# Kernel optimization log

Measured on AMD Instinct MI355X. Metric: run time of the kernel, lower is better.

The kernel has to match this reference:

```python
import jax, jax.numpy as jnp
import numpy as np

B, S, D = 2, 1024, 4096
H, KVH = 32, 8
HD = D // H          # 128
N_REP = H // KVH     # 4
R = 2                # LoRA rank


def setup_inputs() -> dict:
    key = jax.random.key(0)
    ks = jax.random.split(key, 10)
    sc = 0.02
    x = jax.random.normal(ks[0], (B, S, D), jnp.float32)
    wq = jax.random.normal(ks[1], (D, H * HD), jnp.float32) * sc
    wk = jax.random.normal(ks[2], (D, KVH * HD), jnp.float32) * sc
    wv = jax.random.normal(ks[3], (D, KVH * HD), jnp.float32) * sc
    wo = jax.random.normal(ks[4], (H * HD, D), jnp.float32) * sc
    lora_q_a = jax.random.normal(ks[5], (D, R), jnp.float32) * sc
    lora_q_b = jax.random.normal(ks[6], (R, H * HD), jnp.float32) * sc
    lora_v_a = jax.random.normal(ks[7], (D, R), jnp.float32) * sc
    lora_v_b = jax.random.normal(ks[8], (R, KVH * HD), jnp.float32) * sc
    # RoPE frequencies: freqs_cis[t, i] = exp(1j * t * 10000^(-2i/HD))
    inv_freq = 1.0 / (10000.0 ** (jnp.arange(0, HD, 2, dtype=jnp.float32) / HD))  # [HD/2]
    t = jnp.arange(S, dtype=jnp.float32)
    ang = jnp.outer(t, inv_freq)                      # [S, HD/2]
    freqs_cos = jnp.cos(ang)
    freqs_sin = jnp.sin(ang)
    # causal additive mask [1, 1, S, S]
    mask = jnp.triu(jnp.full((S, S), -1e9, jnp.float32), k=1)[None, None]
    return {"x": x, "wq": wq, "wk": wk, "wv": wv, "wo": wo,
            "lora_q_a": lora_q_a, "lora_q_b": lora_q_b,
            "lora_v_a": lora_v_a, "lora_v_b": lora_v_b,
            "freqs_cos": freqs_cos, "freqs_sin": freqs_sin,
            "mask": mask, "start_pos": 0}


def _rope(t, cos, sin):
    # t: [B, S, h, HD]; pairs (even, odd) are (real, imag) of complex halves
    b, s, h, hd = t.shape
    tr = t.reshape(b, s, h, hd // 2, 2)
    a, bb = tr[..., 0], tr[..., 1]
    c = cos[None, :, None, :]
    sn = sin[None, :, None, :]
    out = jnp.stack([a * c - bb * sn, a * sn + bb * c], axis=-1)
    return out.reshape(b, s, h, hd)


def reference(x, wq, wk, wv, wo, lora_q_a, lora_q_b, lora_v_a, lora_v_b,
              freqs_cos, freqs_sin, mask, start_pos):
    # projections + LoRA (note: original Lora_layer applies NO scaling in forward)
    xq = x @ wq + (x @ lora_q_a) @ lora_q_b            # [B,S,H*HD]
    xk = x @ wk                                         # [B,S,KVH*HD]
    xv = x @ wv + (x @ lora_v_a) @ lora_v_b             # [B,S,KVH*HD]
    xq = xq.reshape(B, S, H, HD)
    xk = xk.reshape(B, S, KVH, HD)
    xv = xv.reshape(B, S, KVH, HD)
    xq = _rope(xq, freqs_cos, freqs_sin)
    xk = _rope(xk, freqs_cos, freqs_sin)
    # repeat_kv (GQA expansion): [B,S,KVH,HD] -> [B,S,H,HD]
    k = jnp.repeat(xk, N_REP, axis=2)
    v = jnp.repeat(xv, N_REP, axis=2)
    # attention
    scores = jnp.einsum('bshd,bthd->bhst', xq, k) / np.sqrt(HD).astype(np.float32)
    scores = scores + mask
    probs = jax.nn.softmax(scores.astype(jnp.float32), axis=-1).astype(xq.dtype)
    out = jnp.einsum('bhst,bthd->bshd', probs, v)       # [B,S,H,HD]
    out = out.reshape(B, S, H * HD) @ wo                # [B,S,D]
    return out
```

## Files before the change

kernel.cpp:

```cpp
#include <hip/hip_runtime.h>
#include <stdint.h>

#define B_ 2
#define S_ 1024
#define D_ 4096
#define H_ 32
#define KVH_ 8
#define HD_ 128

typedef short short8 __attribute__((ext_vector_type(8)));
typedef float floatx4 __attribute__((ext_vector_type(4)));

__device__ __forceinline__ ushort f2bf(float f) {
  union { float f; uint32_t u; } v; v.f = f;
  return (ushort)((v.u + 0x7FFFu + ((v.u >> 16) & 1u)) >> 16);
}
__device__ __forceinline__ float bf2f(ushort u) {
  union { uint32_t x; float f; } v; v.x = ((uint32_t)u) << 16; return v.f;
}

__device__ __forceinline__ void gload16(const void* g, void* l) {
  __builtin_amdgcn_global_load_lds((__attribute__((address_space(1))) void*)g,
                                   (__attribute__((address_space(3))) void*)l,
                                   16, 0, 0);
}

__global__ __launch_bounds__(256) void k_cvtlora(const float* __restrict__ x,
                                                 const float* __restrict__ qa,
                                                 const float* __restrict__ va,
                                                 ushort* __restrict__ xb,
                                                 float* __restrict__ xa) {
  const int row = blockIdx.x, t = threadIdx.x;
  const float* xr = x + (size_t)row * D_;
  ushort* xo = xb + (size_t)row * D_;
  float a0 = 0, a1 = 0, a2 = 0, a3 = 0;
#pragma unroll
  for (int it = 0; it < 4; it++) {
    const int i = it * 1024 + t * 4;
    float4 v = *(const float4*)(xr + i);
    ushort o4[4] = {f2bf(v.x), f2bf(v.y), f2bf(v.z), f2bf(v.w)};
    *(uint2*)(xo + i) = *(uint2*)o4;
    float4 q0 = *(const float4*)(qa + 2 * i);
    float4 q1 = *(const float4*)(qa + 2 * i + 4);
    float4 w0 = *(const float4*)(va + 2 * i);
    float4 w1 = *(const float4*)(va + 2 * i + 4);
    a0 += v.x * q0.x + v.y * q0.z + v.z * q1.x + v.w * q1.z;
    a1 += v.x * q0.y + v.y * q0.w + v.z * q1.y + v.w * q1.w;
    a2 += v.x * w0.x + v.y * w0.z + v.z * w1.x + v.w * w1.z;
    a3 += v.x * w0.y + v.y * w0.w + v.z * w1.y + v.w * w1.w;
  }
#pragma unroll
  for (int off = 32; off; off >>= 1) {
    a0 += __shfl_down(a0, off, 64);
    a1 += __shfl_down(a1, off, 64);
    a2 += __shfl_down(a2, off, 64);
    a3 += __shfl_down(a3, off, 64);
  }
  __shared__ float red[4][4];
  const int w = t >> 6, lane = t & 63;
  if (lane == 0) { red[w][0] = a0; red[w][1] = a1; red[w][2] = a2; red[w][3] = a3; }
  __syncthreads();
  if (t < 4)
    xa[(size_t)row * 4 + t] = red[0][t] + red[1][t] + red[2][t] + red[3][t];
}

__global__ __launch_bounds__(256) void k_trw4(const float* __restrict__ wq,
                                              const float* __restrict__ wo,
                                              const float* __restrict__ wk,
                                              const float* __restrict__ wv,
                                              ushort* __restrict__ oq,
                                              ushort* __restrict__ oo,
                                              ushort* __restrict__ ok,
                                              ushort* __restrict__ ov) {
  const int z = blockIdx.z;
  const bool narrow = (z >= 2);
  if (narrow && blockIdx.x >= 16) return;
  const float* in = (z == 0) ? wq : (z == 1) ? wo : (z == 2) ? wk : wv;
  ushort* out = (z == 0) ? oq : (z == 1) ? oo : (z == 2) ? ok : ov;
  const int in_stride = narrow ? 1024 : 4096;
  __shared__ float t[64][65];
  const int n0 = blockIdx.x * 64, k0 = blockIdx.y * 64;
  const int c4 = (threadIdx.x & 15) * 4, r = threadIdx.x >> 4;
#pragma unroll
  for (int rr = 0; rr < 64; rr += 16) {
    float4 v = *(const float4*)&in[(size_t)(k0 + r + rr) * in_stride + n0 + c4];
    t[r + rr][c4] = v.x; t[r + rr][c4 + 1] = v.y;
    t[r + rr][c4 + 2] = v.z; t[r + rr][c4 + 3] = v.w;
  }
  __syncthreads();
#pragma unroll
  for (int rr = 0; rr < 64; rr += 16) {
    const int n = r + rr;
    ushort o4[4] = {f2bf(t[c4][n]), f2bf(t[c4 + 1][n]),
                    f2bf(t[c4 + 2][n]), f2bf(t[c4 + 3][n])};
    *(uint2*)&out[(size_t)(n0 + n) * 4096 + k0 + c4] = *(uint2*)o4;
  }
}

#define GBAR __builtin_amdgcn_s_barrier()
#define VMCNT0 asm volatile("s_waitcnt vmcnt(0)" ::: "memory")
#define VMCNT6 asm volatile("s_waitcnt vmcnt(6)" ::: "memory")

#define QSTG(T, SB) do {                                                     \
    const ushort* ga_ = A + (size_t)(m0 + w * 16 + qsr) * Kz + (T) * 64 + qsc; \
    char* la_ = qlds + (SB) * 65536 + w * 2048;                              \
    gload16(ga_, la_); gload16(ga_ + 8 * Kz, la_ + 1024);                    \
    _Pragma("unroll") for (int u_ = 0; u_ < 3; u_++) {                       \
      const ushort* gb_ = Bt + (size_t)(n0 + u_ * 128 + w * 16 + qsr) * Kz   \
                          + (T) * 64 + qsc;                                  \
      char* lb_ = qlds + (SB) * 65536 + 16384 + u_ * 16384 + w * 2048;       \
      gload16(gb_, lb_); gload16(gb_ + 8 * Kz, lb_ + 1024);                  \
    }                                                                        \
  } while (0)

__global__ __launch_bounds__(512, 2) void k_gemmq(const ushort* __restrict__ A,
                                                  const ushort* __restrict__ Bt,
                                                  ushort* __restrict__ Qb,
                                                  ushort* __restrict__ Kb,
                                                  ushort* __restrict__ Vt,
                                                  const float* __restrict__ xa,
                                                  const float* __restrict__ qb,
                                                  const float* __restrict__ vb,
                                                  const float* __restrict__ fcos,
                                                  const float* __restrict__ fsin) {
  __shared__ char qlds[131072];
  const int flat = blockIdx.y * 16 + blockIdx.x;
  const int swz_id = (flat & 7) * 32 + (flat >> 3);
  const int m0 = (swz_id >> 4) * 128, n0 = (swz_id & 15) * 384;
  const int tid = threadIdx.x, lane = tid & 63, w = tid >> 6;
  const int wr = w >> 2, wc = w & 3;
  const int lr = lane & 15, g = lane >> 4;
  const int swz = (lr & 7) * 16;
  const size_t Kz = 4096;
  const int qsr = lane >> 3;
  const int qsc = ((lane & 7) ^ (qsr & 7)) * 8;

  floatx4 acc[4][6] = {};
  short8 af[4][2], bfr[6][2];

  QSTG(0, 0);
  VMCNT0;
  GBAR;

  for (int t = 0; t < 64; ++t) {
    const int bu = t & 1;
    if (t + 1 < 64) QSTG(t + 1, bu ^ 1);
    const char* ab_ = qlds + bu * 65536 + (wr * 64 + lr) * 128;
#pragma unroll
    for (int fr = 0; fr < 4; fr++)
#pragma unroll
      for (int ks = 0; ks < 2; ks++)
        af[fr][ks] = *(const short8*)(ab_ + fr * 2048 + (((ks * 4 + g) * 16) ^ swz));
    const char* bb_ = qlds + bu * 65536 + 16384 + (wc * 32 + lr) * 128;
#pragma unroll
    for (int u = 0; u < 3; u++)
#pragma unroll
      for (int e = 0; e < 2; e++)
#pragma unroll
        for (int ks = 0; ks < 2; ks++)
          bfr[u * 2 + e][ks] = *(const short8*)(bb_ + u * 16384 + e * 2048 +
                                                (((ks * 4 + g) * 16) ^ swz));
    __builtin_amdgcn_s_setprio(1);
#pragma unroll
    for (int fr = 0; fr < 4; fr++)
#pragma unroll
      for (int u = 0; u < 6; u++)
#pragma unroll
        for (int ks = 0; ks < 2; ks++)
          acc[fr][u] = __builtin_amdgcn_mfma_f32_16x16x32_bf16(
              af[fr][ks], bfr[u][ks], acc[fr][u], 0, 0, 0);
    __builtin_amdgcn_s_setprio(0);
    VMCNT0;
    GBAR;
  }

#pragma unroll
  for (int fr = 0; fr < 4; fr++) {
    const int mb = m0 + wr * 64 + fr * 16 + g * 4;
    const int bb = mb >> 10, s0 = mb & 1023;
    float4 xa4[4];
#pragma unroll
    for (int r = 0; r < 4; r++) xa4[r] = *(const float4*)&xa[(size_t)(mb + r) * 4];
#pragma unroll
    for (int j = 0; j < 3; j++)
#pragma unroll
      for (int e = 0; e < 2; e++) {
        const int n = n0 + j * 128 + wc * 32 + e * 16 + lr;
        if (n < 5120) {
          const bool lq = (n < 4096);
          float b0 = 0.f, b1 = 0.f;
          if (lq) { b0 = qb[n]; b1 = qb[4096 + n]; }
          const int p = (n & 127) >> 1;
          const bool even = !(n & 1);
          const int d = n & 127;
          ushort* dst = lq ? (Qb + ((size_t)(bb * H_ + (n >> 7)) * S_) * HD_ + d)
                           : (Kb + ((size_t)(bb * KVH_ + ((n - 4096) >> 7)) * S_) * HD_ + d);
#pragma unroll
          for (int r = 0; r < 4; r++) {
            float cc = acc[fr][j * 2 + e][r];
            if (lq) cc += xa4[r].x * b0 + xa4[r].y * b1;
            float pv = __shfl_xor(cc, 1, 64);
            const int s = s0 + r;
            float c = fcos[s * 64 + p], sn = fsin[s * 64 + p];
            float o = even ? (cc * c - pv * sn) : (cc * c + pv * sn);
            dst[(size_t)s * HD_] = f2bf(o);
          }
        } else {
          const int vcol = n - 5120;
          const float b0 = vb[vcol], b1 = vb[1024 + vcol];
          ushort v4[4];
#pragma unroll
          for (int r = 0; r < 4; r++)
            v4[r] = f2bf(acc[fr][j * 2 + e][r] + xa4[r].z * b0 + xa4[r].w * b1);
          *(uint2*)&Vt[(size_t)((bb * 8 + (vcol >> 7)) * 128 + (vcol & 127)) * 1024 + s0] =
              *(uint2*)v4;
        }
      }
  }
}

#define OSTG(T, SB) do {                                                     \
    const ushort* ga_ = A + (size_t)(m0 + w * 16 + osr) * Kz + (T) * 64 + osc; \
    char* la_ = olds + (SB) * 49152 + w * 2048;                              \
    gload16(ga_, la_); gload16(ga_ + 8 * Kz, la_ + 1024);                    \
    _Pragma("unroll") for (int u_ = 0; u_ < 2; u_++) {                       \
      const ushort* gb_ = Bt + (size_t)(n0 + u_ * 128 + w * 16 + osr) * Kz + (T) * 64 + osc; \
      char* lb_ = olds + (SB) * 49152 + 16384 + u_ * 16384 + w * 2048;       \
      gload16(gb_, lb_); gload16(gb_ + 8 * Kz, lb_ + 1024);                  \
    }                                                                        \
  } while (0)

#define OTILE(T, RB) do {                                                    \
    if ((T) + 2 < 64) OSTG((T) + 2, ((RB) + 2) % 3);                         \
    const char* ab_ = olds + (RB) * 49152 + (wr * 64 + lr) * 128;            \
    _Pragma("unroll") for (int fr = 0; fr < 4; fr++)                         \
    _Pragma("unroll") for (int ks = 0; ks < 2; ks++)                         \
      af[fr][ks] = *(const short8*)(ab_ + fr * 2048 + (((ks * 4 + g) * 16) ^ swz)); \
    const char* bb_ = olds + (RB) * 49152 + 16384 + (wc * 32 + lr) * 128;    \
    _Pragma("unroll") for (int u_ = 0; u_ < 2; u_++)                         \
    _Pragma("unroll") for (int e_ = 0; e_ < 2; e_++)                         \
    _Pragma("unroll") for (int ks = 0; ks < 2; ks++)                         \
      bfr[u_ * 2 + e_][ks] = *(const short8*)(bb_ + u_ * 16384 + e_ * 2048 + (((ks * 4 + g) * 16) ^ swz)); \
    __builtin_amdgcn_s_setprio(1);                                           \
    _Pragma("unroll") for (int fr = 0; fr < 4; fr++)                         \
    _Pragma("unroll") for (int u_ = 0; u_ < 4; u_++)                         \
    _Pragma("unroll") for (int ks = 0; ks < 2; ks++)                         \
      acc[fr][u_] = __builtin_amdgcn_mfma_f32_16x16x32_bf16(                 \
          af[fr][ks], bfr[u_][ks], acc[fr][u_], 0, 0, 0);                    \
    __builtin_amdgcn_s_setprio(0);                                           \
    if ((T) + 2 < 64) { VMCNT6; } else { VMCNT0; }                           \
    GBAR;                                                                    \
  } while (0)

__global__ __launch_bounds__(512, 2) void k_gemmo(const ushort* __restrict__ A,
                                                  const ushort* __restrict__ Bt,
                                                  float* __restrict__ C) {
  __shared__ char olds[147456];
  const int flat = blockIdx.y * 16 + blockIdx.x;
  const int swz_id = (flat & 7) * 32 + (flat >> 3);
  const int m0 = (swz_id >> 4) * 128, n0 = (swz_id & 15) * 256;
  const int tid = threadIdx.x, lane = tid & 63, w = tid >> 6;
  const int wr = w >> 2, wc = w & 3;
  const int lr = lane & 15, g = lane >> 4;
  const int swz = (lr & 7) * 16;
  const size_t Kz = 4096;
  const int osr = lane >> 3;
  const int osc = ((lane & 7) ^ (osr & 7)) * 8;

  floatx4 acc[4][4] = {};
  short8 af[4][2], bfr[4][2];

  OSTG(0, 0); OSTG(1, 1);
  VMCNT6;
  GBAR;

  for (int tt = 0; tt < 63; tt += 3) {
    OTILE(tt + 0, 0);
    OTILE(tt + 1, 1);
    OTILE(tt + 2, 2);
  }
  OTILE(63, 0);

#pragma unroll
  for (int fr = 0; fr < 4; fr++) {
    const int mb = m0 + wr * 64 + fr * 16 + g * 4;
#pragma unroll
    for (int j = 0; j < 2; j++)
#pragma unroll
      for (int e = 0; e < 2; e++) {
        const int n = n0 + j * 128 + wc * 32 + e * 16 + lr;
#pragma unroll
        for (int r = 0; r < 4; r++)
          C[(size_t)(mb + r) * 4096 + n] = acc[fr][j * 2 + e][r];
      }
  }
}

#define FSTAGE(T, DB) do {                                                   \
    _Pragma("unroll") for (int i_ = 0; i_ < 4; i_++) {                       \
      gload16(Kg + (size_t)((T) * 64 + i_ * 16 + k_srow) * HD_ + k_scol,     \
              fls + (DB) * 16384 + i_ * 4096 + w * 1024);                    \
      gload16(Vg + (size_t)(i_ * 32 + v_srow) * S_ + (T) * 64 + v_scol,      \
              fls + 32768 + (DB) * 16384 + i_ * 4096 + w * 1024);            \
    }                                                                        \
  } while (0)

__global__ __launch_bounds__(256, 2) void k_flash(const ushort* __restrict__ Qb,
                                                  const ushort* __restrict__ Kb,
                                                  const ushort* __restrict__ Vt,
                                                  ushort* __restrict__ attn) {
  __shared__ char fls[81920];
  const int qblk = (gridDim.x - 1) - blockIdx.x;
  const int h = blockIdx.y, b = blockIdx.z;
  const int kvh = h >> 2;
  const int tid = threadIdx.x, w = tid >> 6, lane = tid & 63;
  const int lr = lane & 15, g = lane >> 4;
  const int swz = (lr & 7) * 16;
  const int qra = qblk * 128 + w * 16;
  const ushort* Qrow = Qb + ((size_t)(b * H_ + h) * S_ + qra + lr) * HD_;
  short8 qfa[4], qfb[4];
#pragma unroll
  for (int ks = 0; ks < 4; ks++) {
    qfa[ks] = *(const short8*)(Qrow + ks * 32 + g * 8);
    qfb[ks] = *(const short8*)(Qrow + 64 * HD_ + ks * 32 + g * 8);
  }
  const ushort* Kg = Kb + (size_t)(b * KVH_ + kvh) * S_ * HD_;
  const ushort* Vg = Vt + (size_t)(b * KVH_ + kvh) * HD_ * S_;
  char* Pw = fls + 65536 + w * 4096;
  const int q7 = lr & 7;
  const int k_srow = tid >> 4;
  const int k_scol = ((tid & 15) ^ (k_srow & 7)) * 8;
  const int v_srow = tid >> 3;
  const int v_scol = ((tid & 7) ^ (v_srow & 7)) * 8;
  const float scale = 0.088388347648318447f;

  float m_a = -1e30f, l_a = 0.f, m_b = -1e30f, l_b = 0.f;
  floatx4 oa[8] = {}, ob[8] = {};
  const int nt = 2 * qblk + 2;
  const int lastA = 2 * qblk;

  FSTAGE(0, 0);
  VMCNT0;
  GBAR;

  for (int t = 0; t < nt; t++) {
    const int cur = t & 1;
    if (t + 1 < nt) FSTAGE(t + 1, cur ^ 1);
    const char* Kl = fls + cur * 16384;
    const char* Vl = fls + 32768 + cur * 16384;
    if (t <= lastA) {
      floatx4 s4[4] = {};
      __builtin_amdgcn_s_setprio(1);
#pragma unroll
      for (int mf = 0; mf < 4; mf++) {
        const char* Krow = Kl + (mf * 16 + lr) * 256;
#pragma unroll
        for (int ks = 0; ks < 4; ks++) {
          short8 kf = *(const short8*)(Krow + (((ks * 4 + g) * 16) ^ swz));
          s4[mf] = __builtin_amdgcn_mfma_f32_16x16x32_bf16(kf, qfa[ks], s4[mf], 0, 0, 0);
        }
      }
      __builtin_amdgcn_s_setprio(0);
      float tm = -1e30f;
      if (t == lastA) {
#pragma unroll
        for (int mf = 0; mf < 4; mf++)
#pragma unroll
          for (int r = 0; r < 4; r++) {
            int kv = t * 64 + mf * 16 + g * 4 + r;
            float v = (kv > qra + lr) ? -1e30f : s4[mf][r] * scale;
            s4[mf][r] = v; tm = fmaxf(tm, v);
          }
      } else {
#pragma unroll
        for (int mf = 0; mf < 4; mf++)
#pragma unroll
          for (int r = 0; r < 4; r++) {
            float v = s4[mf][r] * scale;
            s4[mf][r] = v; tm = fmaxf(tm, v);
          }
      }
      tm = fmaxf(tm, __shfl_xor(tm, 16, 64));
      tm = fmaxf(tm, __shfl_xor(tm, 32, 64));
      float m_new = fmaxf(m_a, tm);
      float corr = __expf(m_a - m_new);
      float rs = 0.f;
#pragma unroll
      for (int mf = 0; mf < 4; mf++)
#pragma unroll
        for (int r = 0; r < 4; r++) {
          float p = __expf(s4[mf][r] - m_new);
          s4[mf][r] = p; rs += p;
        }
      rs += __shfl_xor(rs, 16, 64);
      rs += __shfl_xor(rs, 32, 64);
      l_a = l_a * corr + rs; m_a = m_new;
#pragma unroll
      for (int r = 0; r < 4; r++) {
        float cr = __shfl(corr, g * 4 + r, 64);
#pragma unroll
        for (int nf = 0; nf < 8; nf++) oa[nf][r] *= cr;
      }
#pragma unroll
      for (int mf = 0; mf < 4; mf++) {
        uint2 pv;
        pv.x = (uint32_t)f2bf(s4[mf][0]) | ((uint32_t)f2bf(s4[mf][1]) << 16);
        pv.y = (uint32_t)f2bf(s4[mf][2]) | ((uint32_t)f2bf(s4[mf][3]) << 16);
        *(uint2*)(Pw + lr * 128 + ((mf * 32 + g * 8) ^ (q7 << 4))) = pv;
      }
    }
    {
      floatx4 s4[4] = {};
      __builtin_amdgcn_s_setprio(1);
#pragma unroll
      for (int mf = 0; mf < 4; mf++) {
        const char* Krow = Kl + (mf * 16 + lr) * 256;
#pragma unroll
        for (int ks = 0; ks < 4; ks++) {
          short8 kf = *(const short8*)(Krow + (((ks * 4 + g) * 16) ^ swz));
          s4[mf] = __builtin_amdgcn_mfma_f32_16x16x32_bf16(kf, qfb[ks], s4[mf], 0, 0, 0);
        }
      }
      __builtin_amdgcn_s_setprio(0);
      float tm = -1e30f;
      if (t == nt - 1) {
#pragma unroll
        for (int mf = 0; mf < 4; mf++)
#pragma unroll
          for (int r = 0; r < 4; r++) {
            int kv = t * 64 + mf * 16 + g * 4 + r;
            float v = (kv > qra + 64 + lr) ? -1e30f : s4[mf][r] * scale;
            s4[mf][r] = v; tm = fmaxf(tm, v);
          }
      } else {
#pragma unroll
        for (int mf = 0; mf < 4; mf++)
#pragma unroll
          for (int r = 0; r < 4; r++) {
            float v = s4[mf][r] * scale;
            s4[mf][r] = v; tm = fmaxf(tm, v);
          }
      }
      tm = fmaxf(tm, __shfl_xor(tm, 16, 64));
      tm = fmaxf(tm, __shfl_xor(tm, 32, 64));
      float m_new = fmaxf(m_b, tm);
      float corr = __expf(m_b - m_new);
      float rs = 0.f;
#pragma unroll
      for (int mf = 0; mf < 4; mf++)
#pragma unroll
        for (int r = 0; r < 4; r++) {
          float p = __expf(s4[mf][r] - m_new);
          s4[mf][r] = p; rs += p;
        }
      rs += __shfl_xor(rs, 16, 64);
      rs += __shfl_xor(rs, 32, 64);
      l_b = l_b * corr + rs; m_b = m_new;
#pragma unroll
      for (int r = 0; r < 4; r++) {
        float cr = __shfl(corr, g * 4 + r, 64);
#pragma unroll
        for (int nf = 0; nf < 8; nf++) ob[nf][r] *= cr;
      }
#pragma unroll
      for (int mf = 0; mf < 4; mf++) {
        uint2 pv;
        pv.x = (uint32_t)f2bf(s4[mf][0]) | ((uint32_t)f2bf(s4[mf][1]) << 16);
        pv.y = (uint32_t)f2bf(s4[mf][2]) | ((uint32_t)f2bf(s4[mf][3]) << 16);
        *(uint2*)(Pw + 2048 + lr * 128 + ((mf * 32 + g * 8) ^ (q7 << 4))) = pv;
      }
    }
    __builtin_amdgcn_s_setprio(1);
#pragma unroll
    for (int ks2 = 0; ks2 < 2; ks2++) {
      short8 pb = *(const short8*)(Pw + 2048 + lr * 128 + ((ks2 * 64 + g * 16) ^ (q7 << 4)));
      short8 pa = pb;
      if (t <= lastA)
        pa = *(const short8*)(Pw + lr * 128 + ((ks2 * 64 + g * 16) ^ (q7 << 4)));
#pragma unroll
      for (int nf = 0; nf < 8; nf++) {
        short8 vf = *(const short8*)(Vl + (nf * 16 + lr) * 128 + (((ks2 * 4 + g) * 16) ^ swz));
        if (t <= lastA)
          oa[nf] = __builtin_amdgcn_mfma_f32_16x16x32_bf16(pa, vf, oa[nf], 0, 0, 0);
        ob[nf] = __builtin_amdgcn_mfma_f32_16x16x32_bf16(pb, vf, ob[nf], 0, 0, 0);
      }
    }
    __builtin_amdgcn_s_setprio(0);
    VMCNT0;
    GBAR;
  }
  const float linva = 1.0f / l_a, linvb = 1.0f / l_b;
  ushort* outp = attn + ((size_t)(b * S_) + qra) * 4096 + h * 128;
#pragma unroll
  for (int r = 0; r < 4; r++) {
    float lia = __shfl(linva, g * 4 + r, 64);
    float lib = __shfl(linvb, g * 4 + r, 64);
    ushort* orow = outp + (size_t)(g * 4 + r) * 4096;
#pragma unroll
    for (int nf = 0; nf < 8; nf++) {
      orow[nf * 16 + lr] = f2bf(oa[nf][r] * lia);
      orow[(size_t)64 * 4096 + nf * 16 + lr] = f2bf(ob[nf][r] * lib);
    }
  }
}

extern "C" void kernel_launch(void* const* d_in, const int* in_sizes, int n_in,
                              void* d_out, int out_size, void* d_ws, size_t ws_size,
                              hipStream_t stream) {
  (void)in_sizes; (void)n_in; (void)out_size; (void)ws_size;
  const float* x    = (const float*)d_in[0];
  const float* wq   = (const float*)d_in[1];
  const float* wk   = (const float*)d_in[2];
  const float* wv   = (const float*)d_in[3];
  const float* wo   = (const float*)d_in[4];
  const float* lqa  = (const float*)d_in[5];
  const float* lqb  = (const float*)d_in[6];
  const float* lva  = (const float*)d_in[7];
  const float* lvb  = (const float*)d_in[8];
  const float* fcos = (const float*)d_in[9];
  const float* fsin = (const float*)d_in[10];

  char* ws = (char*)d_ws;
  ushort* xb   = (ushort*)(ws + 0);
  ushort* wT   = (ushort*)(ws + 16777216);
  ushort* woT  = (ushort*)(ws + 67108864);
  ushort* Qb   = (ushort*)(ws + 150994944);
  ushort* Kb   = (ushort*)(ws + 167772160);
  ushort* Vt   = (ushort*)(ws + 171966464);
  ushort* attn = (ushort*)(ws + 176160768);
  float*  xa   = (float*) (ws + 192937984);

  k_cvtlora<<<2048, 256, 0, stream>>>(x, lqa, lva, xb, xa);
  k_trw4<<<dim3(64, 64, 4), 256, 0, stream>>>(
      wq, wo, wk, wv, wT, woT,
      wT + (size_t)4096 * 4096, wT + (size_t)5120 * 4096);
  k_gemmq<<<dim3(16, 16), 512, 0, stream>>>(xb, wT, Qb, Kb, Vt, xa, lqb, lvb,
                                            fcos, fsin);
  k_flash<<<dim3(8, 32, 2), 256, 0, stream>>>(Qb, Kb, Vt, attn);
  k_gemmo<<<dim3(16, 16), 512, 0, stream>>>(attn, woT, (float*)d_out);
}
```

Baseline: 291.8 us.

## Merge x-convert/LoRA into weight-transpose launch; double-buffer output GEMM

Folds the x-to-bf16 conversion and LoRA down-projection kernel into the weight transpose kernel as an extra grid z-slice, removing one launch and letting both run concurrently. Separately, the output projection GEMM goes from a triple-buffered LDS pipeline with partial vmcnt waits to a double-buffered one that waits for all loads each iteration. This cuts LDS from 144KB to 96KB per block, but the full vmcnt(0) wait exposes more global-load latency, because the prefetch is only one tile ahead.

```diff
diff --git a/kernel.cpp b/kernel.cpp
--- a/kernel.cpp
+++ b/kernel.cpp
@@ -25,54 +25,57 @@
                                    16, 0, 0);
 }
 
-__global__ __launch_bounds__(256) void k_cvtlora(const float* __restrict__ x,
-                                                 const float* __restrict__ qa,
-                                                 const float* __restrict__ va,
-                                                 ushort* __restrict__ xb,
-                                                 float* __restrict__ xa) {
-  const int row = blockIdx.x, t = threadIdx.x;
-  const float* xr = x + (size_t)row * D_;
-  ushort* xo = xb + (size_t)row * D_;
-  float a0 = 0, a1 = 0, a2 = 0, a3 = 0;
-#pragma unroll
-  for (int it = 0; it < 4; it++) {
-    const int i = it * 1024 + t * 4;
-    float4 v = *(const float4*)(xr + i);
-    ushort o4[4] = {f2bf(v.x), f2bf(v.y), f2bf(v.z), f2bf(v.w)};
-    *(uint2*)(xo + i) = *(uint2*)o4;
-    float4 q0 = *(const float4*)(qa + 2 * i);
-    float4 q1 = *(const float4*)(qa + 2 * i + 4);
-    float4 w0 = *(const float4*)(va + 2 * i);
-    float4 w1 = *(const float4*)(va + 2 * i + 4);
-    a0 += v.x * q0.x + v.y * q0.z + v.z * q1.x + v.w * q1.z;
-    a1 += v.x * q0.y + v.y * q0.w + v.z * q1.y + v.w * q1.w;
-    a2 += v.x * w0.x + v.y * w0.z + v.z * w1.x + v.w * w1.z;
-    a3 += v.x * w0.y + v.y * w0.w + v.z * w1.y + v.w * w1.w;
-  }
-#pragma unroll
-  for (int off = 32; off; off >>= 1) {
-    a0 += __shfl_down(a0, off, 64);
-    a1 += __shfl_down(a1, off, 64);
-    a2 += __shfl_down(a2, off, 64);
-    a3 += __shfl_down(a3, off, 64);
-  }
-  __shared__ float red[4][4];
-  const int w = t >> 6, lane = t & 63;
-  if (lane == 0) { red[w][0] = a0; red[w][1] = a1; red[w][2] = a2; red[w][3] = a3; }
-  __syncthreads();
-  if (t < 4)
-    xa[(size_t)row * 4 + t] = red[0][t] + red[1][t] + red[2][t] + red[3][t];
-}
-
-__global__ __launch_bounds__(256) void k_trw4(const float* __restrict__ wq,
+__global__ __launch_bounds__(256) void k_prep(const float* __restrict__ wq,
                                               const float* __restrict__ wo,
                                               const float* __restrict__ wk,
                                               const float* __restrict__ wv,
                                               ushort* __restrict__ oq,
                                               ushort* __restrict__ oo,
                                               ushort* __restrict__ ok,
-                                              ushort* __restrict__ ov) {
+                                              ushort* __restrict__ ov,
+                                              const float* __restrict__ x,
+                                              const float* __restrict__ qa,
+                                              const float* __restrict__ va,
+                                              ushort* __restrict__ xb,
+                                              float* __restrict__ xa) {
   const int z = blockIdx.z;
+  if (z == 4) {
+    const int row = blockIdx.y * 64 + blockIdx.x;
+    if (row >= 2048) return;
+    const int t = threadIdx.x;
+    const float* xr = x + (size_t)row * D_;
+    ushort* xo = xb + (size_t)row * D_;
+    float a0 = 0, a1 = 0, a2 = 0, a3 = 0;
+#pragma unroll
+    for (int it = 0; it < 4; it++) {
+      const int i = it * 1024 + t * 4;
+      float4 v = *(const float4*)(xr + i);
+      ushort o4[4] = {f2bf(v.x), f2bf(v.y), f2bf(v.z), f2bf(v.w)};
+      *(uint2*)(xo + i) = *(uint2*)o4;
+      float4 q0 = *(const float4*)(qa + 2 * i);
+      float4 q1 = *(const float4*)(qa + 2 * i + 4);
+      float4 w0 = *(const float4*)(va + 2 * i);
+      float4 w1 = *(const float4*)(va + 2 * i + 4);
+      a0 += v.x * q0.x + v.y * q0.z + v.z * q1.x + v.w * q1.z;
+      a1 += v.x * q0.y + v.y * q0.w + v.z * q1.y + v.w * q1.w;
+      a2 += v.x * w0.x + v.y * w0.z + v.z * w1.x + v.w * w1.z;
+      a3 += v.x * w0.y + v.y * w0.w + v.z * w1.y + v.w * w1.w;
+    }
+#pragma unroll
+    for (int off = 32; off; off >>= 1) {
+      a0 += __shfl_down(a0, off, 64);
+      a1 += __shfl_down(a1, off, 64);
+      a2 += __shfl_down(a2, off, 64);
+      a3 += __shfl_down(a3, off, 64);
+    }
+    __shared__ float red[4][4];
+    const int w = t >> 6, lane = t & 63;
+    if (lane == 0) { red[w][0] = a0; red[w][1] = a1; red[w][2] = a2; red[w][3] = a3; }
+    __syncthreads();
+    if (t < 4)
+      xa[(size_t)row * 4 + t] = red[0][t] + red[1][t] + red[2][t] + red[3][t];
+    return;
+  }
   const bool narrow = (z >= 2);
   if (narrow && blockIdx.x >= 16) return;
   const float* in = (z == 0) ? wq : (z == 1) ? wo : (z == 2) ? wk : wv;
@@ -99,7 +102,6 @@
 
 #define GBAR __builtin_amdgcn_s_barrier()
 #define VMCNT0 asm volatile("s_waitcnt vmcnt(0)" ::: "memory")
-#define VMCNT6 asm volatile("s_waitcnt vmcnt(6)" ::: "memory")
 
 #define QSTG(T, SB) do {                                                     \
     const ushort* ga_ = A + (size_t)(m0 + w * 16 + qsr) * Kz + (T) * 64 + qsc; \
@@ -230,32 +232,10 @@
     }                                                                        \
   } while (0)
 
-#define OTILE(T, RB) do {                                                    \
-    if ((T) + 2 < 64) OSTG((T) + 2, ((RB) + 2) % 3);                         \
-    const char* ab_ = olds + (RB) * 49152 + (wr * 64 + lr) * 128;            \
-    _Pragma("unroll") for (int fr = 0; fr < 4; fr++)                         \
-    _Pragma("unroll") for (int ks = 0; ks < 2; ks++)                         \
-      af[fr][ks] = *(const short8*)(ab_ + fr * 2048 + (((ks * 4 + g) * 16) ^ swz)); \
-    const char* bb_ = olds + (RB) * 49152 + 16384 + (wc * 32 + lr) * 128;    \
-    _Pragma("unroll") for (int u_ = 0; u_ < 2; u_++)                         \
-    _Pragma("unroll") for (int e_ = 0; e_ < 2; e_++)                         \
-    _Pragma("unroll") for (int ks = 0; ks < 2; ks++)                         \
-      bfr[u_ * 2 + e_][ks] = *(const short8*)(bb_ + u_ * 16384 + e_ * 2048 + (((ks * 4 + g) * 16) ^ swz)); \
-    __builtin_amdgcn_s_setprio(1);                                           \
-    _Pragma("unroll") for (int fr = 0; fr < 4; fr++)                         \
-    _Pragma("unroll") for (int u_ = 0; u_ < 4; u_++)                         \
-    _Pragma("unroll") for (int ks = 0; ks < 2; ks++)                         \
-      acc[fr][u_] = __builtin_amdgcn_mfma_f32_16x16x32_bf16(                 \
-          af[fr][ks], bfr[u_][ks], acc[fr][u_], 0, 0, 0);                    \
-    __builtin_amdgcn_s_setprio(0);                                           \
-    if ((T) + 2 < 64) { VMCNT6; } else { VMCNT0; }                           \
-    GBAR;                                                                    \
-  } while (0)
-
 __global__ __launch_bounds__(512, 2) void k_gemmo(const ushort* __restrict__ A,
                                                   const ushort* __restrict__ Bt,
                                                   float* __restrict__ C) {
-  __shared__ char olds[147456];
+  __shared__ char olds[98304];
   const int flat = blockIdx.y * 16 + blockIdx.x;
   const int swz_id = (flat & 7) * 32 + (flat >> 3);
   const int m0 = (swz_id >> 4) * 128, n0 = (swz_id & 15) * 256;
@@ -270,16 +250,41 @@
   floatx4 acc[4][4] = {};
   short8 af[4][2], bfr[4][2];
 
-  OSTG(0, 0); OSTG(1, 1);
-  VMCNT6;
+  OSTG(0, 0);
+  VMCNT0;
   GBAR;
 
-  for (int tt = 0; tt < 63; tt += 3) {
-    OTILE(tt + 0, 0);
-    OTILE(tt + 1, 1);
-    OTILE(tt + 2, 2);
-  }
-  OTILE(63, 0);
+  for (int t = 0; t < 64; ++t) {
+    const int bu = t & 1;
+    if (t + 1 < 64) OSTG(t + 1, bu ^ 1);
+    const char* ab_ = olds + bu * 49152 + (wr * 64 + lr) * 128;
+#pragma unroll
+    for (int fr = 0; fr < 4; fr++)
+#pragma unroll
+      for (int ks = 0; ks < 2; ks++)
+        af[fr][ks] = *(const short8*)(ab_ + fr * 2048 + (((ks * 4 + g) * 16) ^ swz));
+    const char* bb_ = olds + bu * 49152 + 16384 + (wc * 32 + lr) * 128;
+#pragma unroll
+    for (int u = 0; u < 2; u++)
+#pragma unroll
+      for (int e = 0; e < 2; e++)
+#pragma unroll
+        for (int ks = 0; ks < 2; ks++)
+          bfr[u * 2 + e][ks] = *(const short8*)(bb_ + u * 16384 + e * 2048 +
+                                                (((ks * 4 + g) * 16) ^ swz));
+    __builtin_amdgcn_s_setprio(1);
+#pragma unroll
+    for (int fr = 0; fr < 4; fr++)
+#pragma unroll
+      for (int u = 0; u < 4; u++)
+#pragma unroll
+        for (int ks = 0; ks < 2; ks++)
+          acc[fr][u] = __builtin_amdgcn_mfma_f32_16x16x32_bf16(
+              af[fr][ks], bfr[u][ks], acc[fr][u], 0, 0, 0);
+    __builtin_amdgcn_s_setprio(0);
+    VMCNT0;
+    GBAR;
+  }
 
 #pragma unroll
   for (int fr = 0; fr < 4; fr++) {
@@ -530,10 +535,10 @@
   ushort* attn = (ushort*)(ws + 176160768);
   float*  xa   = (float*) (ws + 192937984);
 
-  k_cvtlora<<<2048, 256, 0, stream>>>(x, lqa, lva, xb, xa);
-  k_trw4<<<dim3(64, 64, 4), 256, 0, stream>>>(
+  k_prep<<<dim3(64, 64, 5), 256, 0, stream>>>(
       wq, wo, wk, wv, wT, woT,
-      wT + (size_t)4096 * 4096, wT + (size_t)5120 * 4096);
+      wT + (size_t)4096 * 4096, wT + (size_t)5120 * 4096,
+      x, lqa, lva, xb, xa);
   k_gemmq<<<dim3(16, 16), 512, 0, stream>>>(xb, wT, Qb, Kb, Vt, xa, lqb, lvb,
                                             fcos, fsin);
   k_flash<<<dim3(8, 32, 2), 256, 0, stream>>>(Qb, Kb, Vt, attn);
```

After: 294.4 us. Within noise of the previous version (+0.9%).
